# Optimization experiments

Hardware: AMD Instinct MI355X
Metric: run time of the kernel (lower is better)

Reference implementation:

```python
import jax, jax.numpy as jnp
import numpy as np

M, N, D, H, R = 16384, 32, 128, 8, 237
Dh = D // H
SCALE = Dh ** -0.5
LN_EPS = 1e-5


def setup_inputs() -> dict:
    key = jax.random.key(0)
    ks = jax.random.split(key, 12)
    entity_repr = jax.random.normal(ks[0], (M, D), dtype=jnp.float32)
    neighbor_index = jax.random.randint(ks[1], (M, N), 0, M, dtype=jnp.int64)
    rel_ids = jax.random.randint(ks[2], (M, N), 0, R, dtype=jnp.int64)
    neighbor_mask = jax.random.randint(ks[3], (M, N), 0, 2, dtype=jnp.int32).astype(bool)
    neighbor_mask = neighbor_mask.at[:, 0].set(True)  # ensure >=1 valid neighbor per node
    s = 1.0 / np.sqrt(D)
    # weights stored in right-multiply form: y = x @ W + b
    Wq = jax.random.normal(ks[4], (D, D), dtype=jnp.float32) * s
    Wk = jax.random.normal(ks[5], (D, D), dtype=jnp.float32) * s
    Wv = jax.random.normal(ks[6], (D, D), dtype=jnp.float32) * s
    Wo = jax.random.normal(ks[7], (D, D), dtype=jnp.float32) * s
    bq = jnp.zeros((D,), jnp.float32)
    bk = jnp.zeros((D,), jnp.float32)
    bv = jnp.zeros((D,), jnp.float32)
    bo = jnp.zeros((D,), jnp.float32)
    rel_table = jax.random.normal(ks[8], (R, D), dtype=jnp.float32)
    ln_gamma = jnp.ones((D,), jnp.float32)
    ln_beta = jnp.zeros((D,), jnp.float32)
    return {
        "entity_repr": entity_repr, "neighbor_index": neighbor_index,
        "rel_ids": rel_ids, "neighbor_mask": neighbor_mask,
        "Wq": Wq, "bq": bq, "Wk": Wk, "bk": bk, "Wv": Wv, "bv": bv,
        "Wo": Wo, "bo": bo, "rel_table": rel_table,
        "ln_gamma": ln_gamma, "ln_beta": ln_beta,
    }


def _layernorm(x, gamma, beta):
    mu = jnp.mean(x, axis=-1, keepdims=True)
    var = jnp.var(x, axis=-1, keepdims=True)
    return (x - mu) * jax.lax.rsqrt(var + LN_EPS) * gamma + beta


def reference(entity_repr, neighbor_index, rel_ids, neighbor_mask,
              Wq, bq, Wk, bk, Wv, bv, Wo, bo, rel_table, ln_gamma, ln_beta):
    valid = neighbor_mask
    safe_index = jnp.where(valid, neighbor_index, 0)
    safe_rel = jnp.where(valid, rel_ids, 0)
    neighbor_repr = entity_repr[safe_index]          # [M, N, D] irregular gather
    rel_emb = rel_table[safe_rel]                     # [M, N, D]
    q = (entity_repr @ Wq + bq).reshape(M, H, Dh)     # [M, H, Dh] (query len 1)
    k = ((neighbor_repr + rel_emb) @ Wk + bk).reshape(M, N, H, Dh)
    v = (neighbor_repr @ Wv + bv).reshape(M, N, H, Dh)
    attn = jnp.einsum("mhd,mnhd->mhn", q, k) * SCALE  # [M, H, N]
    attn = jnp.where(valid[:, None, :], attn, -jnp.inf)
    attn = jax.nn.softmax(attn, axis=-1)
    attn = jnp.nan_to_num(attn, nan=0.0)
    out = jnp.einsum("mhn,mnhd->mhd", attn, v).reshape(M, D)
    out = out @ Wo + bo
    return _layernorm(entity_repr + out, ln_gamma, ln_beta)
```

## Files before the change

### kernel.cpp

```cpp
#include <hip/hip_runtime.h>

#define M_NODES 16384
#define NNBR 32
#define RREL 237
#define ATTN_SCALE 0.25f
#define LN_EPS 1e-5f

typedef float float4v __attribute__((ext_vector_type(4)));
typedef unsigned int uint4v __attribute__((ext_vector_type(4)));
typedef short short8 __attribute__((ext_vector_type(8)));
typedef float floatx4 __attribute__((ext_vector_type(4)));

__device__ __forceinline__ float bfu2f(unsigned short u) {
    return __builtin_bit_cast(float, ((unsigned int)u) << 16);
}
__device__ __forceinline__ unsigned short f2bfu(float f) {
    unsigned int x = __builtin_bit_cast(unsigned int, f);
    unsigned int lsb = (x >> 16) & 1u;
    x += 0x7fffu + lsb;
    return (unsigned short)(x >> 16);
}
__device__ __forceinline__ unsigned int pack2(float a, float b) {
    return (unsigned int)f2bfu(a) | ((unsigned int)f2bfu(b) << 16);
}
__device__ __forceinline__ float unpk_lo(unsigned int u) {
    return __builtin_bit_cast(float, u << 16);
}
__device__ __forceinline__ float unpk_hi(unsigned int u) {
    return __builtin_bit_cast(float, u & 0xffff0000u);
}


__global__ __launch_bounds__(256) void prep_w(
    const float* __restrict__ Wq, const float* __restrict__ Wk,
    const float* __restrict__ Wv, const float* __restrict__ Wo,
    const float* __restrict__ entity,
    unsigned short* __restrict__ WqT, unsigned short* __restrict__ WkT,
    unsigned short* __restrict__ WvT, unsigned short* __restrict__ WoT,
    unsigned short* __restrict__ Eb) {
    int t = threadIdx.x;
    if (blockIdx.x < 32) {
        int mat  = blockIdx.x >> 3;
        int slab = blockIdx.x & 7;
        const float* W = (mat == 0) ? Wq : (mat == 1) ? Wk : (mat == 2) ? Wv : Wo;
        unsigned short* WT = (mat == 0) ? WqT : (mat == 1) ? WkT : (mat == 2) ? WvT : WoT;
        #pragma unroll
        for (int i = 0; i < 8; ++i) {
            int idx = t + 256 * i;
            int r = slab * 16 + (idx >> 7);
            int c = idx & 127;
            WT[c * 128 + r] = f2bfu(W[r * 128 + c]);
        }
    } else {
        int b = blockIdx.x - 32;
        const float* src = entity + (size_t)b * 16384;
        unsigned short* dst = Eb + (size_t)b * 16384;
        #pragma unroll
        for (int i = 0; i < 8; ++i) {
            int o = (i * 256 + t) * 8;
            float4v f0 = *(const float4v*)&src[o];
            float4v f1 = *(const float4v*)&src[o + 4];
            short8 s;
            #pragma unroll
            for (int j = 0; j < 4; ++j) {
                s[j]     = (short)f2bfu(f0[j]);
                s[4 + j] = (short)f2bfu(f1[j]);
            }
            *(short8*)&dst[o] = s;
        }
    }
}

__global__ __launch_bounds__(256) void gemm4_mfma(
    const float* __restrict__ rel_table, const unsigned short* __restrict__ Eb,
    const unsigned short* __restrict__ WqT, const unsigned short* __restrict__ WkT,
    const unsigned short* __restrict__ WvT,
    const float* __restrict__ bq, const float* __restrict__ bk,
    const float* __restrict__ bv,
    unsigned short* __restrict__ EQb, unsigned short* __restrict__ EKV,
    unsigned short* __restrict__ RKb) {
    __shared__ __align__(16) unsigned short lw[128 * 136];

    int y = blockIdx.y;
    const unsigned short* WT; const float* bias; int arows;
    unsigned short* outb; int ostride, ooff;
    if (y == 0)      { WT = WqT; bias = bq;      arows = M_NODES; outb = EQb; ostride = 128; ooff = 0;   }
    else if (y == 1) { WT = WkT; bias = nullptr; arows = M_NODES; outb = EKV; ostride = 256; ooff = 0;   }
    else if (y == 2) { WT = WvT; bias = bv;      arows = M_NODES; outb = EKV; ostride = 256; ooff = 128; }
    else             { WT = WkT; bias = bk;      arows = RREL;    outb = RKb; ostride = 128; ooff = 0;   }

    int rbase = blockIdx.x * 64;
    if (rbase >= arows) return;
    int t = threadIdx.x;
    int wave = t >> 6, lane = t & 63;
    int lm = lane & 15, quad = lane >> 4;
    int m0 = rbase + wave * 16;
    int r0 = m0 + lm; if (r0 >= arows) r0 = arows - 1;

    short8 af[4];
    if (y == 3) {
        #pragma unroll
        for (int ks = 0; ks < 4; ++ks) {
            int koff = ks * 32 + quad * 8;
            float4v f0 = *(const float4v*)&rel_table[r0 * 128 + koff];
            float4v f1 = *(const float4v*)&rel_table[r0 * 128 + koff + 4];
            #pragma unroll
            for (int j = 0; j < 4; ++j) {
                af[ks][j]     = (short)f2bfu(f0[j]);
                af[ks][4 + j] = (short)f2bfu(f1[j]);
            }
        }
    } else {
        #pragma unroll
        for (int ks = 0; ks < 4; ++ks)
            af[ks] = *(const short8*)&Eb[r0 * 128 + ks * 32 + quad * 8];
    }

    #pragma unroll
    for (int i = 0; i < 8; ++i) {
        int ci = t + 256 * i;
        int r  = ci >> 4;
        int c8 = ci & 15;
        *(short8*)&lw[r * 136 + c8 * 8] = *(const short8*)&WT[r * 128 + c8 * 8];
    }
    __syncthreads();

    floatx4 acc[8];
    #pragma unroll
    for (int c = 0; c < 8; ++c) acc[c] = (floatx4){0.f, 0.f, 0.f, 0.f};

    #pragma unroll
    for (int ks = 0; ks < 4; ++ks) {
        int koff = ks * 32 + quad * 8;
        #pragma unroll
        for (int c = 0; c < 8; ++c) {
            short8 b = *(const short8*)&lw[(c * 16 + lm) * 136 + koff];
            acc[c] = __builtin_amdgcn_mfma_f32_16x16x32_bf16(af[ks], b, acc[c], 0, 0, 0);
        }
    }

    #pragma unroll
    for (int c = 0; c < 8; ++c) {
        int col = c * 16 + lm;
        float bb = bias ? bias[col] : 0.0f;
        int rb = m0 + quad * 4;
        #pragma unroll
        for (int j = 0; j < 4; ++j) {
            int r = rb + j;
            if (r < arows) outb[r * ostride + ooff + col] = f2bfu(acc[c][j] + bb);
        }
    }
}

__global__ __launch_bounds__(256) void attn_gather(
    const int* __restrict__ nidx, const int* __restrict__ nrel,
    const int* __restrict__ nmask,
    const unsigned short* __restrict__ EQb, const unsigned short* __restrict__ EKV,
    const unsigned short* __restrict__ RKb,
    unsigned short* __restrict__ OATb) {
    __shared__ float Pl[4][8][33];

    int w = threadIdx.x >> 6, l = threadIdx.x & 63;
    int m = blockIdx.x * 4 + w;
    int lm = l & 15, quad = l >> 4;
    int n0 = l & 31;

    short8 q8v[4];
    #pragma unroll
    for (int ks = 0; ks < 4; ++ks)
        q8v[ks] = *(const short8*)&EQb[m * 128 + ks * 32 + quad * 8];

    int mk = nmask[m * NNBR + n0];
    int ix = nidx[m * NNBR + n0];
    int ir = nrel[m * NNBR + n0];
    if (!mk) { ix = 0; ir = 0; }
    ix = ix < 0 ? 0 : (ix > M_NODES - 1 ? M_NODES - 1 : ix);
    ir = ir < 0 ? 0 : (ir > RREL - 1 ? RREL - 1 : ir);
    unsigned long long bal = __ballot(mk != 0);
    unsigned maskbits = (unsigned)(bal & 0xffffffffu);

    short8 vreg[8];
    #pragma unroll
    for (int i = 0; i < 8; ++i) {
        int ixx = __shfl(ix, quad + i * 4, 64);
        vreg[i] = *(const short8*)&EKV[ixx * 256 + 128 + lm * 8];
    }

    int rowK0 = __shfl(ix, lm, 64),      rowK1 = __shfl(ix, 16 + lm, 64);
    int rowR0 = __shfl(ir, lm, 64),      rowR1 = __shfl(ir, 16 + lm, 64);

    floatx4 acc0 = (floatx4){0.f, 0.f, 0.f, 0.f};
    floatx4 acc1 = (floatx4){0.f, 0.f, 0.f, 0.f};
    const short8 zero8 = (short8){0, 0, 0, 0, 0, 0, 0, 0};
    #pragma unroll
    for (int ks = 0; ks < 4; ++ks) {
        int koff = ks * 32 + quad * 8;
        int h = ks * 2 + (quad >> 1);
        short8 bq = (lm == h) ? q8v[ks] : zero8;
        short8 k0 = *(const short8*)&EKV[rowK0 * 256 + koff];
        short8 k1 = *(const short8*)&EKV[rowK1 * 256 + koff];
        short8 r0 = *(const short8*)&RKb[rowR0 * 128 + koff];
        short8 r1 = *(const short8*)&RKb[rowR1 * 128 + koff];
        acc0 = __builtin_amdgcn_mfma_f32_16x16x32_bf16(k0, bq, acc0, 0, 0, 0);
        acc0 = __builtin_amdgcn_mfma_f32_16x16x32_bf16(r0, bq, acc0, 0, 0, 0);
        acc1 = __builtin_amdgcn_mfma_f32_16x16x32_bf16(k1, bq, acc1, 0, 0, 0);
        acc1 = __builtin_amdgcn_mfma_f32_16x16x32_bf16(r1, bq, acc1, 0, 0, 0);
    }

    float lf[2][4];
    #pragma unroll
    for (int j = 0; j < 4; ++j) {
        int na = quad * 4 + j, nb = 16 + quad * 4 + j;
        float va = acc0[j] * ATTN_SCALE;
        float vb = acc1[j] * ATTN_SCALE;
        lf[0][j] = ((maskbits >> na) & 1) ? va : -1e30f;
        lf[1][j] = ((maskbits >> nb) & 1) ? vb : -1e30f;
    }
    float mx = -1e30f;
    #pragma unroll
    for (int g = 0; g < 2; ++g)
        #pragma unroll
        for (int j = 0; j < 4; ++j) mx = fmaxf(mx, lf[g][j]);
    mx = fmaxf(mx, __shfl_xor(mx, 16, 64));
    mx = fmaxf(mx, __shfl_xor(mx, 32, 64));
    float p[2][4];
    float s = 0.f;
    #pragma unroll
    for (int g = 0; g < 2; ++g)
        #pragma unroll
        for (int j = 0; j < 4; ++j) { p[g][j] = __expf(lf[g][j] - mx); s += p[g][j]; }
    s += __shfl_xor(s, 16, 64);
    s += __shfl_xor(s, 32, 64);
    float inv = 1.0f / s;
    if (lm < 8) {
        #pragma unroll
        for (int g = 0; g < 2; ++g)
            #pragma unroll
            for (int j = 0; j < 4; ++j)
                Pl[w][lm][g * 16 + quad * 4 + j] = p[g][j] * inv;
    }

    float o[8] = {0.f, 0.f, 0.f, 0.f, 0.f, 0.f, 0.f, 0.f};
    #pragma unroll
    for (int i = 0; i < 8; ++i) {
        float pp = Pl[w][lm >> 1][quad + i * 4];
        #pragma unroll
        for (int j = 0; j < 8; ++j) o[j] += pp * bfu2f((unsigned short)vreg[i][j]);
    }
    #pragma unroll
    for (int j = 0; j < 8; ++j) {
        o[j] += __shfl_xor(o[j], 16, 64);
        o[j] += __shfl_xor(o[j], 32, 64);
    }
    if (quad == 0) {
        uint4v u;
        u[0] = pack2(o[0], o[1]); u[1] = pack2(o[2], o[3]);
        u[2] = pack2(o[4], o[5]); u[3] = pack2(o[6], o[7]);
        *(uint4v*)&OATb[m * 128 + lm * 8] = u;
    }
}

__global__ __launch_bounds__(256) void gemm_wo_ln(
    const unsigned short* __restrict__ OATb, const unsigned short* __restrict__ WoT,
    const float* __restrict__ bo, const float* __restrict__ entity,
    const float* __restrict__ gamma_, const float* __restrict__ beta_,
    float* __restrict__ OUT) {
    __shared__ __align__(16) unsigned short lw[128 * 136];

    int t = threadIdx.x;
    int wave = t >> 6, lane = t & 63;
    int lm = lane & 15, quad = lane >> 4;
    int m0 = blockIdx.x * 64 + wave * 16;
    int r0 = m0 + lm;

    short8 af[4];
    #pragma unroll
    for (int ks = 0; ks < 4; ++ks)
        af[ks] = *(const short8*)&OATb[r0 * 128 + ks * 32 + quad * 8];

    #pragma unroll
    for (int i = 0; i < 8; ++i) {
        int ci = t + 256 * i;
        int r  = ci >> 4;
        int c8 = ci & 15;
        *(short8*)&lw[r * 136 + c8 * 8] = *(const short8*)&WoT[r * 128 + c8 * 8];
    }
    __syncthreads();

    floatx4 acc[8];
    #pragma unroll
    for (int c = 0; c < 8; ++c) acc[c] = (floatx4){0.f, 0.f, 0.f, 0.f};

    #pragma unroll
    for (int ks = 0; ks < 4; ++ks) {
        int koff = ks * 32 + quad * 8;
        #pragma unroll
        for (int c = 0; c < 8; ++c) {
            short8 b = *(const short8*)&lw[(c * 16 + lm) * 136 + koff];
            acc[c] = __builtin_amdgcn_mfma_f32_16x16x32_bf16(af[ks], b, acc[c], 0, 0, 0);
        }
    }

    float bb[8], gg[8], be[8];
    #pragma unroll
    for (int c = 0; c < 8; ++c) {
        int col = c * 16 + lm;
        bb[c] = bo[col]; gg[c] = gamma_[col]; be[c] = beta_[col];
    }
    #pragma unroll
    for (int j = 0; j < 4; ++j) {
        int r = m0 + quad * 4 + j;
        float y[8];
        float s1 = 0.f, s2 = 0.f;
        #pragma unroll
        for (int c = 0; c < 8; ++c) {
            float v = acc[c][j] + bb[c] + entity[r * 128 + c * 16 + lm];
            y[c] = v; s1 += v; s2 += v * v;
        }
        #pragma unroll
        for (int off = 8; off >= 1; off >>= 1) {
            s1 += __shfl_xor(s1, off, 16);
            s2 += __shfl_xor(s2, off, 16);
        }
        float mu  = s1 * (1.0f / 128.0f);
        float var = fmaxf(s2 * (1.0f / 128.0f) - mu * mu, 0.0f);
        float rs  = rsqrtf(var + LN_EPS);
        #pragma unroll
        for (int c = 0; c < 8; ++c)
            OUT[r * 128 + c * 16 + lm] = (y[c] - mu) * rs * gg[c] + be[c];
    }
}

__global__ __launch_bounds__(256, 6) void rga_fused(
    const float* __restrict__ entity,
    const int* __restrict__ nidx,
    const int* __restrict__ nrel,
    const int* __restrict__ nmask,
    const float* __restrict__ Wq, const float* __restrict__ bq,
    const float* __restrict__ Wk, const float* __restrict__ bk,
    const float* __restrict__ Wv, const float* __restrict__ bv,
    const float* __restrict__ Wo, const float* __restrict__ bo,
    const float* __restrict__ rel_table,
    const float* __restrict__ gamma_, const float* __restrict__ beta_,
    float* __restrict__ outp) {
    __shared__ __align__(16) float er[128];
    __shared__ __align__(16) float qv[128];
    __shared__ float qb[8];
    __shared__ __align__(16) float qk[8 * 132];
    __shared__ __align__(16) unsigned int nbvp[32 * 68];
    __shared__ float Lg[8][33];
    __shared__ __align__(16) float pv[8 * 132];
    __shared__ __align__(16) float oat[128];
    __shared__ float ypart[2][128];
    __shared__ float red[4];
    __shared__ int midx[32], mrel[32], mmask[32];

    int m = blockIdx.x;
    int t = threadIdx.x;

    if (t < 32) {
        int mk = nmask[m * NNBR + t];
        int ix = nidx[m * NNBR + t];
        int ir = nrel[m * NNBR + t];
        if (!mk) { ix = 0; ir = 0; }
        ix = ix < 0 ? 0 : (ix > M_NODES - 1 ? M_NODES - 1 : ix);
        ir = ir < 0 ? 0 : (ir > RREL - 1 ? RREL - 1 : ir);
        mmask[t] = mk; midx[t] = ix; mrel[t] = ir;
    }
    if (t >= 128) er[t - 128] = entity[m * 128 + (t - 128)];
    __syncthreads();

    {
        int half = t >> 7, d = t & 127, j0 = half * 64;
        const float4v* e4 = (const float4v*)&er[j0];
        float acc = 0.f;
        #pragma unroll 4
        for (int c = 0; c < 16; ++c) {
            float4v ev = e4[c];
            #pragma unroll
            for (int k = 0; k < 4; ++k)
                acc += ev[k] * Wq[(j0 + c * 4 + k) * 128 + d];
        }
        ypart[half][d] = acc;
    }
    __syncthreads();
    if (t < 128) qv[t] = ypart[0][t] + ypart[1][t] + bq[t];
    __syncthreads();

    #pragma unroll
    for (int rep = 0; rep < 4; ++rep) {
        int o = rep * 256 + t;
        int h = o >> 7, j = o & 127;
        const float4v* wr = (const float4v*)&Wk[j * 128 + h * 16];
        const float4v* q4 = (const float4v*)&qv[h * 16];
        float s = 0.f;
        #pragma unroll
        for (int c = 0; c < 4; ++c) {
            float4v ww = wr[c], q = q4[c];
            #pragma unroll
            for (int k = 0; k < 4; ++k) s += ww[k] * q[k];
        }
        qk[h * 132 + j] = s;
    }
    if (t < 8) {
        float s = 0.f;
        #pragma unroll
        for (int dh = 0; dh < 16; ++dh) s += qv[t * 16 + dh] * bk[t * 16 + dh];
        qb[t] = s;
    }
    __syncthreads();

    {
        int n = t >> 3, c16 = t & 7, j0 = c16 * 16;
        int ix = midx[n], ir = mrel[n];
        const float4v* ep = (const float4v*)&entity[ix * 128 + j0];
        const float4v* rp = (const float4v*)&rel_table[ir * 128 + j0];
        float ev[16], kv[16];
        #pragma unroll
        for (int c = 0; c < 4; ++c) {
            float4v e4 = ep[c], r4 = rp[c];
            #pragma unroll
            for (int k = 0; k < 4; ++k) {
                ev[c * 4 + k] = e4[k];
                kv[c * 4 + k] = e4[k] + r4[k];
            }
        }
        uint4v u0, u1;
        #pragma unroll
        for (int k = 0; k < 4; ++k) u0[k] = pack2(ev[2 * k], ev[2 * k + 1]);
        #pragma unroll
        for (int k = 0; k < 4; ++k) u1[k] = pack2(ev[8 + 2 * k], ev[9 + 2 * k]);
        *(uint4v*)&nbvp[n * 68 + c16 * 8]     = u0;
        *(uint4v*)&nbvp[n * 68 + c16 * 8 + 4] = u1;
        float acc[8];
        #pragma unroll
        for (int h = 0; h < 8; ++h) {
            const float4v* qrow = (const float4v*)&qk[h * 132 + j0];
            float s = 0.f;
            #pragma unroll
            for (int c = 0; c < 4; ++c) {
                float4v q = qrow[c];
                #pragma unroll
                for (int k = 0; k < 4; ++k) s += q[k] * kv[c * 4 + k];
            }
            acc[h] = s;
        }
        #pragma unroll
        for (int off = 1; off < 8; off <<= 1) {
            #pragma unroll
            for (int h = 0; h < 8; ++h) acc[h] += __shfl_xor(acc[h], off, 8);
        }
        if (c16 == 0) {
            #pragma unroll
            for (int h = 0; h < 8; ++h) {
                float lf = (acc[h] + qb[h]) * ATTN_SCALE;
                if (!mmask[n]) lf = -1e30f;
                Lg[h][n] = lf;
            }
        }
    }
    __syncthreads();

    {
        int h = t >> 5, n = t & 31;
        float lf = Lg[h][n];
        float mx = lf;
        #pragma unroll
        for (int off = 16; off >= 1; off >>= 1) mx = fmaxf(mx, __shfl_xor(mx, off, 32));
        float p = __expf(lf - mx);
        float s = p;
        #pragma unroll
        for (int off = 16; off >= 1; off >>= 1) s += __shfl_xor(s, off, 32);
        Lg[h][n] = p / s;
    }
    __syncthreads();

    {
        int h = t >> 5, c4 = t & 31;
        float4v a = (float4v){0.f, 0.f, 0.f, 0.f};
        #pragma unroll 8
        for (int n = 0; n < 32; ++n) {
            float p = Lg[h][n];
            unsigned int w0 = nbvp[n * 68 + c4 * 2];
            unsigned int w1 = nbvp[n * 68 + c4 * 2 + 1];
            a[0] += p * unpk_lo(w0);
            a[1] += p * unpk_hi(w0);
            a[2] += p * unpk_lo(w1);
            a[3] += p * unpk_hi(w1);
        }
        *(float4v*)&pv[h * 132 + c4 * 4] = a;
    }
    __syncthreads();

    {
        int half = t >> 7, d = t & 127, j0 = half * 64;
        int h = d >> 4;
        const float4v* p4 = (const float4v*)&pv[h * 132 + j0];
        float acc = 0.f;
        #pragma unroll 4
        for (int c = 0; c < 16; ++c) {
            float4v p = p4[c];
            #pragma unroll
            for (int k = 0; k < 4; ++k)
                acc += p[k] * Wv[(j0 + c * 4 + k) * 128 + d];
        }
        ypart[half][d] = acc;
    }
    __syncthreads();
    if (t < 128) oat[t] = ypart[0][t] + ypart[1][t] + bv[t];
    __syncthreads();

    {
        int half = t >> 7, d = t & 127, j0 = half * 64;
        const float4v* o4 = (const float4v*)&oat[j0];
        float acc = 0.f;
        #pragma unroll 4
        for (int c = 0; c < 16; ++c) {
            float4v o = o4[c];
            #pragma unroll
            for (int k = 0; k < 4; ++k)
                acc += o[k] * Wo[(j0 + c * 4 + k) * 128 + d];
        }
        ypart[half][d] = acc;
    }
    __syncthreads();

    float x = 0.f;
    if (t < 128) {
        x = er[t] + ypart[0][t] + ypart[1][t] + bo[t];
        float s1 = x, s2 = x * x;
        #pragma unroll
        for (int off = 32; off >= 1; off >>= 1) {
            s1 += __shfl_xor(s1, off, 64);
            s2 += __shfl_xor(s2, off, 64);
        }
        if ((t & 63) == 0) { red[(t >> 6) * 2] = s1; red[(t >> 6) * 2 + 1] = s2; }
    }
    __syncthreads();
    if (t < 128) {
        float mu  = (red[0] + red[2]) * (1.0f / 128.0f);
        float ms  = (red[1] + red[3]) * (1.0f / 128.0f);
        float var = fmaxf(ms - mu * mu, 0.0f);
        float rs  = rsqrtf(var + LN_EPS);
        outp[m * 128 + t] = (x - mu) * rs * gamma_[t] + beta_[t];
    }
}

extern "C" void kernel_launch(void* const* d_in, const int* in_sizes, int n_in,
                              void* d_out, int out_size, void* d_ws, size_t ws_size,
                              hipStream_t stream) {
    const float* entity    = (const float*)d_in[0];
    const int*   nidx      = (const int*)d_in[1];
    const int*   nrel      = (const int*)d_in[2];
    const int*   nmask     = (const int*)d_in[3];
    const float* Wq        = (const float*)d_in[4];
    const float* bq        = (const float*)d_in[5];
    const float* Wk        = (const float*)d_in[6];
    const float* bk        = (const float*)d_in[7];
    const float* Wv        = (const float*)d_in[8];
    const float* bv        = (const float*)d_in[9];
    const float* Wo        = (const float*)d_in[10];
    const float* bo        = (const float*)d_in[11];
    const float* rel_table = (const float*)d_in[12];
    const float* gamma_    = (const float*)d_in[13];
    const float* beta_     = (const float*)d_in[14];

    char* ws = (char*)d_ws;
    unsigned short* EKV  = (unsigned short*)(ws + 0);
    unsigned short* EQb  = (unsigned short*)(ws + 8388608);
    unsigned short* OATb = (unsigned short*)(ws + 12582912);
    unsigned short* RKb  = (unsigned short*)(ws + 16777216);
    unsigned short* WqT  = (unsigned short*)(ws + 16837888);
    unsigned short* WkT  = (unsigned short*)(ws + 16870656);
    unsigned short* WvT  = (unsigned short*)(ws + 16903424);
    unsigned short* WoT  = (unsigned short*)(ws + 16936192);
    unsigned short* Eb   = (unsigned short*)(ws + 16968960);
    const size_t NEED = 16968960 + 4194304;

    if (ws_size >= NEED) {
        prep_w<<<dim3(160), 256, 0, stream>>>(Wq, Wk, Wv, Wo, entity,
                                              WqT, WkT, WvT, WoT, Eb);
        gemm4_mfma<<<dim3(256, 4), 256, 0, stream>>>(
            rel_table, Eb, WqT, WkT, WvT, bq, bk, bv, EQb, EKV, RKb);
        attn_gather<<<dim3(M_NODES / 4), 256, 0, stream>>>(
            nidx, nrel, nmask, EQb, EKV, RKb, OATb);
        gemm_wo_ln<<<dim3(256), 256, 0, stream>>>(
            OATb, WoT, bo, entity, gamma_, beta_, (float*)d_out);
    } else {
        rga_fused<<<dim3(M_NODES), 256, 0, stream>>>(
            entity, nidx, nrel, nmask, Wq, bq, Wk, bk, Wv, bv, Wo, bo,
            rel_table, gamma_, beta_, (float*)d_out);
    }
}
```

Before: 137.5 us.

## Fuse Q/K/V projections per row tile and read weights directly from global/L2

Restructures the projection GEMM so each block loads its bf16 entity A-fragments once and runs the Q, K and V projections in sequence, instead of launching a separate block per weight matrix. Weight B-fragments are now read straight from global memory (expected to hit in cache) rather than staged through LDS with a barrier, in both the QKV kernel and the Wo+LayerNorm kernel. Blocks shrink to 128 threads with 512+8 blocks. This removes the LDS staging, the sync and the repeated A loads, but in exchange it relies on L1/L2 hits for the weight reads, which are strided across rows.

```diff
diff --git a/kernel.cpp b/kernel.cpp
--- a/kernel.cpp
+++ b/kernel.cpp
@@ -71,7 +71,36 @@
     }
 }
 
-__global__ __launch_bounds__(256) void gemm4_mfma(
+__device__ __forceinline__ void mm16(
+    const short8* af, const unsigned short* __restrict__ WT,
+    const float* __restrict__ bias, unsigned short* __restrict__ outb,
+    int ostride, int ooff, int m0, int arows, int lm, int quad) {
+    floatx4 acc[8];
+    #pragma unroll
+    for (int c = 0; c < 8; ++c) acc[c] = (floatx4){0.f, 0.f, 0.f, 0.f};
+    #pragma unroll
+    for (int ks = 0; ks < 4; ++ks) {
+        int koff = ks * 32 + quad * 8;
+        #pragma unroll
+        for (int c = 0; c < 8; ++c) {
+            short8 b = *(const short8*)&WT[(c * 16 + lm) * 128 + koff];
+            acc[c] = __builtin_amdgcn_mfma_f32_16x16x32_bf16(af[ks], b, acc[c], 0, 0, 0);
+        }
+    }
+    #pragma unroll
+    for (int c = 0; c < 8; ++c) {
+        int col = c * 16 + lm;
+        float bb = bias ? bias[col] : 0.0f;
+        int rb = m0 + quad * 4;
+        #pragma unroll
+        for (int j = 0; j < 4; ++j) {
+            int r = rb + j;
+            if (r < arows) outb[r * ostride + ooff + col] = f2bfu(acc[c][j] + bb);
+        }
+    }
+}
+
+__global__ __launch_bounds__(128) void gemm_qkv(
     const float* __restrict__ rel_table, const unsigned short* __restrict__ Eb,
     const unsigned short* __restrict__ WqT, const unsigned short* __restrict__ WkT,
     const unsigned short* __restrict__ WvT,
@@ -79,26 +108,25 @@
     const float* __restrict__ bv,
     unsigned short* __restrict__ EQb, unsigned short* __restrict__ EKV,
     unsigned short* __restrict__ RKb) {
-    __shared__ __align__(16) unsigned short lw[128 * 136];
-
-    int y = blockIdx.y;
-    const unsigned short* WT; const float* bias; int arows;
-    unsigned short* outb; int ostride, ooff;
-    if (y == 0)      { WT = WqT; bias = bq;      arows = M_NODES; outb = EQb; ostride = 128; ooff = 0;   }
-    else if (y == 1) { WT = WkT; bias = nullptr; arows = M_NODES; outb = EKV; ostride = 256; ooff = 0;   }
-    else if (y == 2) { WT = WvT; bias = bv;      arows = M_NODES; outb = EKV; ostride = 256; ooff = 128; }
-    else             { WT = WkT; bias = bk;      arows = RREL;    outb = RKb; ostride = 128; ooff = 0;   }
-
-    int rbase = blockIdx.x * 64;
-    if (rbase >= arows) return;
     int t = threadIdx.x;
     int wave = t >> 6, lane = t & 63;
     int lm = lane & 15, quad = lane >> 4;
-    int m0 = rbase + wave * 16;
-    int r0 = m0 + lm; if (r0 >= arows) r0 = arows - 1;
-
-    short8 af[4];
-    if (y == 3) {
+    int bx = blockIdx.x;
+
+    if (bx < 512) {
+        int m0 = bx * 32 + wave * 16;
+        int r0 = m0 + lm;
+        short8 af[4];
+        #pragma unroll
+        for (int ks = 0; ks < 4; ++ks)
+            af[ks] = *(const short8*)&Eb[r0 * 128 + ks * 32 + quad * 8];
+        mm16(af, WqT, bq,      EQb, 128, 0,   m0, M_NODES, lm, quad);
+        mm16(af, WkT, nullptr, EKV, 256, 0,   m0, M_NODES, lm, quad);
+        mm16(af, WvT, bv,      EKV, 256, 128, m0, M_NODES, lm, quad);
+    } else {
+        int m0 = (bx - 512) * 32 + wave * 16;
+        int r0 = m0 + lm; if (r0 >= RREL) r0 = RREL - 1;
+        short8 af[4];
         #pragma unroll
         for (int ks = 0; ks < 4; ++ks) {
             int koff = ks * 32 + quad * 8;
@@ -110,45 +138,7 @@
                 af[ks][4 + j] = (short)f2bfu(f1[j]);
             }
         }
-    } else {
-        #pragma unroll
-        for (int ks = 0; ks < 4; ++ks)
-            af[ks] = *(const short8*)&Eb[r0 * 128 + ks * 32 + quad * 8];
-    }
-
-    #pragma unroll
-    for (int i = 0; i < 8; ++i) {
-        int ci = t + 256 * i;
-        int r  = ci >> 4;
-        int c8 = ci & 15;
-        *(short8*)&lw[r * 136 + c8 * 8] = *(const short8*)&WT[r * 128 + c8 * 8];
-    }
-    __syncthreads();
-
-    floatx4 acc[8];
-    #pragma unroll
-    for (int c = 0; c < 8; ++c) acc[c] = (floatx4){0.f, 0.f, 0.f, 0.f};
-
-    #pragma unroll
-    for (int ks = 0; ks < 4; ++ks) {
-        int koff = ks * 32 + quad * 8;
-        #pragma unroll
-        for (int c = 0; c < 8; ++c) {
-            short8 b = *(const short8*)&lw[(c * 16 + lm) * 136 + koff];
-            acc[c] = __builtin_amdgcn_mfma_f32_16x16x32_bf16(af[ks], b, acc[c], 0, 0, 0);
-        }
-    }
-
-    #pragma unroll
-    for (int c = 0; c < 8; ++c) {
-        int col = c * 16 + lm;
-        float bb = bias ? bias[col] : 0.0f;
-        int rb = m0 + quad * 4;
-        #pragma unroll
-        for (int j = 0; j < 4; ++j) {
-            int r = rb + j;
-            if (r < arows) outb[r * ostride + ooff + col] = f2bfu(acc[c][j] + bb);
-        }
+        mm16(af, WkT, bk, RKb, 128, 0, m0, RREL, lm, quad);
     }
 }
 
@@ -265,8 +255,6 @@
     const float* __restrict__ bo, const float* __restrict__ entity,
     const float* __restrict__ gamma_, const float* __restrict__ beta_,
     float* __restrict__ OUT) {
-    __shared__ __align__(16) unsigned short lw[128 * 136];
-
     int t = threadIdx.x;
     int wave = t >> 6, lane = t & 63;
     int lm = lane & 15, quad = lane >> 4;
@@ -278,15 +266,6 @@
     for (int ks = 0; ks < 4; ++ks)
         af[ks] = *(const short8*)&OATb[r0 * 128 + ks * 32 + quad * 8];
 
-    #pragma unroll
-    for (int i = 0; i < 8; ++i) {
-        int ci = t + 256 * i;
-        int r  = ci >> 4;
-        int c8 = ci & 15;
-        *(short8*)&lw[r * 136 + c8 * 8] = *(const short8*)&WoT[r * 128 + c8 * 8];
-    }
-    __syncthreads();
-
     floatx4 acc[8];
     #pragma unroll
     for (int c = 0; c < 8; ++c) acc[c] = (floatx4){0.f, 0.f, 0.f, 0.f};
@@ -296,7 +275,7 @@
         int koff = ks * 32 + quad * 8;
         #pragma unroll
         for (int c = 0; c < 8; ++c) {
-            short8 b = *(const short8*)&lw[(c * 16 + lm) * 136 + koff];
+            short8 b = *(const short8*)&WoT[(c * 16 + lm) * 128 + koff];
             acc[c] = __builtin_amdgcn_mfma_f32_16x16x32_bf16(af[ks], b, acc[c], 0, 0, 0);
         }
     }
@@ -580,7 +559,7 @@
     if (ws_size >= NEED) {
         prep_w<<<dim3(160), 256, 0, stream>>>(Wq, Wk, Wv, Wo, entity,
                                               WqT, WkT, WvT, WoT, Eb);
-        gemm4_mfma<<<dim3(256, 4), 256, 0, stream>>>(
+        gemm_qkv<<<dim3(520), 128, 0, stream>>>(
             rel_table, Eb, WqT, WkT, WvT, bq, bk, bv, EQb, EKV, RKb);
         attn_gather<<<dim3(M_NODES / 4), 256, 0, stream>>>(
             nidx, nrel, nmask, EQb, EKV, RKb, OATb);
```

After: 156.2 us. 1.14x slower.
